# Performance work log

Hardware: AMD Instinct MI355X
Metric: run time of the kernel (lower is better)

Reference implementation:

```python
import jax, jax.numpy as jnp
import numpy as np

B, T, S = 256, 32, 128
I, H, O = 256, 1024, 256


def setup_inputs() -> dict:
    key = jax.random.key(0)
    ks = jax.random.split(key, 8)
    sc = 0.02
    return {
        "shifted_target": jax.random.normal(ks[0], (B, T, I), jnp.float32),
        "encoder_outputs": jax.random.normal(ks[1], (B, S, H), jnp.float32),
        "W_ih": jax.random.normal(ks[2], (4 * H, I), jnp.float32) * sc,
        "W_hh": jax.random.normal(ks[3], (4 * H, H), jnp.float32) * sc,
        "b_ih": jax.random.normal(ks[4], (4 * H,), jnp.float32) * sc,
        "b_hh": jax.random.normal(ks[5], (4 * H,), jnp.float32) * sc,
        "W_fc": jax.random.normal(ks[6], (O, 2 * H), jnp.float32) * sc,
        "b_fc": jax.random.normal(ks[7], (O,), jnp.float32) * sc,
    }


def reference(shifted_target, encoder_outputs, W_ih, W_hh, b_ih, b_hh, W_fc, b_fc):
    bs, tgt_len, inp = shifted_target.shape
    hid = encoder_outputs.shape[-1]
    # torch code feeds zeros (not shifted_target[:,0]) at t=0, with zero init state
    xs = shifted_target.at[:, 0, :].set(0.0)
    xs = jnp.swapaxes(xs, 0, 1)  # [T, B, I]

    def step(carry, x_t):
        h, c = carry
        gates = x_t @ W_ih.T + b_ih + h @ W_hh.T + b_hh  # [B, 4H]
        i, f, g, o = jnp.split(gates, 4, axis=-1)
        i = jax.nn.sigmoid(i)
        f = jax.nn.sigmoid(f)
        g = jnp.tanh(g)
        o = jax.nn.sigmoid(o)
        c = f * c + i * g
        h = o * jnp.tanh(c)
        # dot-product attention against encoder states
        score = jnp.einsum('bh,bsh->bs', h, encoder_outputs)
        prob = jax.nn.softmax(score, axis=-1)
        ctx = jnp.einsum('bs,bsh->bh', prob, encoder_outputs)
        out_t = jnp.concatenate([ctx, h], axis=-1) @ W_fc.T + b_fc
        return (h, c), (out_t, prob)

    h0 = jnp.zeros((bs, hid), shifted_target.dtype)
    c0 = jnp.zeros((bs, hid), shifted_target.dtype)
    _, (outs, probs) = jax.lax.scan(step, (h0, c0), xs)
    return jnp.swapaxes(outs, 0, 1), jnp.swapaxes(probs, 0, 1)
```

## Files before the change

kernel.cpp:

```cpp
#include <hip/hip_runtime.h>
#include <math.h>

#define B_  256
#define T_  32
#define S_  128
#define I_  256
#define H_  1024
#define O_  256
#define G4  4096
#define K2  2048

typedef __attribute__((ext_vector_type(8))) short bf16x8;
typedef __attribute__((ext_vector_type(4))) float f32x4;

#define MFMA16(a, b, c) __builtin_amdgcn_mfma_f32_16x16x32_bf16(a, b, c, 0, 0, 0)

__device__ __forceinline__ unsigned short f2bf(float f) {
    unsigned int u = __float_as_uint(f);
    u = (u + 0x7FFFu + ((u >> 16) & 1u)) >> 16;
    return (unsigned short)u;
}
__device__ __forceinline__ unsigned int pack2(float a, float b) {
    return (unsigned int)f2bf(a) | ((unsigned int)f2bf(b) << 16);
}
__device__ __forceinline__ float sigm(float x) { return 1.0f / (1.0f + __expf(-x)); }

__global__ void prep_kernel(
    const float* __restrict__ x, const float* __restrict__ Wih,
    const float* __restrict__ Whh, const float* __restrict__ bih,
    const float* __restrict__ bhh, const float* __restrict__ Wfc,
    unsigned short* __restrict__ WihR, unsigned short* __restrict__ WhhR,
    unsigned short* __restrict__ WfcR, float* __restrict__ biasR,
    unsigned short* __restrict__ xs, unsigned short* __restrict__ h0,
    unsigned short* __restrict__ h1, float* __restrict__ c)
{
    const long NWHH = (long)G4 * H_;
    const long NWIH = (long)G4 * I_;
    const long NWFC = (long)O_ * K2;
    const long NB   = G4;
    const long NX   = (long)B_ * T_ * I_;
    const long NH   = (long)B_ * H_;
    const long total = NWHH + NWIH + NWFC + NB + NX + 3 * NH;
    for (long i = (long)blockIdx.x * blockDim.x + threadIdx.x; i < total;
         i += (long)gridDim.x * blockDim.x) {
        long j = i;
        if (j < NWHH) {
            int r = (int)(j >> 10), k = (int)(j & 1023);
            int n = ((r & 1023) << 2) | (r >> 10);
            WhhR[(long)n * H_ + k] = f2bf(Whh[j]);
            continue;
        }
        j -= NWHH;
        if (j < NWIH) {
            int r = (int)(j >> 8), k = (int)(j & 255);
            int n = ((r & 1023) << 2) | (r >> 10);
            WihR[(long)n * I_ + k] = f2bf(Wih[j]);
            continue;
        }
        j -= NWIH;
        if (j < NWFC) { WfcR[j] = f2bf(Wfc[j]); continue; }
        j -= NWFC;
        if (j < NB) {
            int r = (int)j;
            int n = ((r & 1023) << 2) | (r >> 10);
            biasR[n] = bih[r] + bhh[r];
            continue;
        }
        j -= NB;
        if (j < NX) {
            int t = (int)((j >> 8) & 31);
            xs[j] = (t == 0) ? (unsigned short)0 : f2bf(x[j]);
            continue;
        }
        j -= NX;
        if (j < NH) { h0[j] = 0; continue; }
        j -= NH;
        if (j < NH) { h1[j] = 0; continue; }
        j -= NH;
        c[j] = 0.0f;
    }
}

__global__ __launch_bounds__(256) void step_kernel(
    const unsigned short* __restrict__ xs,
    const unsigned short* __restrict__ WihR,
    const unsigned short* __restrict__ WhhR,
    const float* __restrict__ biasR,
    const unsigned short* __restrict__ hprev,
    unsigned short* __restrict__ hnext,
    float* __restrict__ c,
    unsigned short* __restrict__ hall,
    int t)
{
    __shared__ __align__(16) char smem[64 * 132 * 4];
    unsigned short* As = (unsigned short*)smem;
    unsigned short* Bs = (unsigned short*)(smem + 64 * 40 * 2);
    float* Gs = (float*)smem;

    const int tid = threadIdx.x;
    const int lane = tid & 63, wave = tid >> 6;
    const int wm = wave >> 1, wn = wave & 1;
    const int quad = lane >> 4, l16 = lane & 15;
    const int n0 = blockIdx.x * 128, m0 = blockIdx.y * 64;

    const int arow = tid >> 2, akc = (tid & 3) * 8;
    const int brow = tid >> 1, bkc = (tid & 1) * 16;

    f32x4 acc[2][4];
    const f32x4 z = {0.f, 0.f, 0.f, 0.f};
#pragma unroll
    for (int i = 0; i < 2; i++)
#pragma unroll
        for (int j = 0; j < 4; j++) acc[i][j] = z;

    for (int k0 = 0; k0 < I_ + H_; k0 += 32) {
        {
            int kg = k0 + akc;
            const unsigned short* src = (kg < I_)
                ? xs + ((long)(m0 + arow) * T_ + t) * I_ + kg
                : hprev + (long)(m0 + arow) * H_ + (kg - I_);
            *(uint4*)(As + arow * 40 + akc) = *(const uint4*)src;
        }
        {
            int kg = k0 + bkc;
            const unsigned short* src = (kg < I_)
                ? WihR + (long)(n0 + brow) * I_ + kg
                : WhhR + (long)(n0 + brow) * H_ + (kg - I_);
            *(uint4*)(Bs + brow * 40 + bkc)     = *(const uint4*)src;
            *(uint4*)(Bs + brow * 40 + bkc + 8) = *(const uint4*)(src + 8);
        }
        __syncthreads();
        bf16x8 a0 = *(const bf16x8*)(As + (wm * 32 + l16) * 40 + quad * 8);
        bf16x8 a1 = *(const bf16x8*)(As + (wm * 32 + 16 + l16) * 40 + quad * 8);
#pragma unroll
        for (int j = 0; j < 4; j++) {
            bf16x8 bb = *(const bf16x8*)(Bs + (wn * 64 + j * 16 + l16) * 40 + quad * 8);
            acc[0][j] = MFMA16(a0, bb, acc[0][j]);
            acc[1][j] = MFMA16(a1, bb, acc[1][j]);
        }
        __syncthreads();
    }
#pragma unroll
    for (int i = 0; i < 2; i++)
#pragma unroll
        for (int j = 0; j < 4; j++)
#pragma unroll
            for (int r = 0; r < 4; r++) {
                int row = wm * 32 + i * 16 + quad * 4 + r;
                int col = wn * 64 + j * 16 + l16;
                Gs[row * 132 + col] = acc[i][j][r] + biasR[n0 + col];
            }
    __syncthreads();
    for (int p = tid; p < 2048; p += 256) {
        int row = p >> 5, u = p & 31;
        float gi = Gs[row * 132 + u * 4 + 0];
        float gf = Gs[row * 132 + u * 4 + 1];
        float gg = Gs[row * 132 + u * 4 + 2];
        float go = Gs[row * 132 + u * 4 + 3];
        int b = m0 + row;
        int jg = (n0 >> 2) + u;
        float ii = sigm(gi), ff = sigm(gf), g3 = tanhf(gg), oo = sigm(go);
        float cn = ff * c[(long)b * H_ + jg] + ii * g3;
        float hh = oo * tanhf(cn);
        c[(long)b * H_ + jg] = cn;
        unsigned short hb = f2bf(hh);
        hnext[(long)b * H_ + jg] = hb;
        hall[((long)b * T_ + t) * H_ + jg] = hb;
    }
}

__global__ __launch_bounds__(256) void attn_kernel(
    const float* __restrict__ enc,
    const unsigned short* __restrict__ hall,
    float* __restrict__ probs,
    unsigned short* __restrict__ cat)
{
    __shared__ __align__(16) unsigned short As2[32 * 72];
    __shared__ __align__(16) unsigned short Bs2[128 * 72];
    __shared__ __align__(16) float Sc[32 * 132];

    const int tid = threadIdx.x;
    const int lane = tid & 63, wave = tid >> 6;
    const int mw = wave & 1, nw = wave >> 1;
    const int quad = lane >> 4, l16 = lane & 15;
    const int b = blockIdx.x;

    f32x4 acc[4];
    const f32x4 z = {0.f, 0.f, 0.f, 0.f};
#pragma unroll
    for (int j = 0; j < 4; j++) acc[j] = z;

    const int arow = tid >> 3, akc = (tid & 7) * 8;
    const int brow = tid >> 1, bkc = (tid & 1) * 32;

    for (int k0 = 0; k0 < H_; k0 += 64) {
        *(uint4*)(As2 + arow * 72 + akc) =
            *(const uint4*)(hall + ((long)b * T_ + arow) * H_ + k0 + akc);
        {
            const float* ep = enc + ((long)b * S_ + brow) * H_ + k0 + bkc;
#pragma unroll
            for (int i = 0; i < 4; i++) {
                float4 f0 = *(const float4*)(ep + i * 8);
                float4 f1 = *(const float4*)(ep + i * 8 + 4);
                uint4 v;
                v.x = pack2(f0.x, f0.y);
                v.y = pack2(f0.z, f0.w);
                v.z = pack2(f1.x, f1.y);
                v.w = pack2(f1.z, f1.w);
                *(uint4*)(Bs2 + brow * 72 + bkc + i * 8) = v;
            }
        }
        __syncthreads();
#pragma unroll
        for (int ks = 0; ks < 2; ks++) {
            bf16x8 a = *(const bf16x8*)(As2 + (mw * 16 + l16) * 72 + ks * 32 + quad * 8);
#pragma unroll
            for (int j = 0; j < 4; j++) {
                bf16x8 bb = *(const bf16x8*)(Bs2 + (nw * 64 + j * 16 + l16) * 72 + ks * 32 + quad * 8);
                acc[j] = MFMA16(a, bb, acc[j]);
            }
        }
        __syncthreads();
    }
#pragma unroll
    for (int j = 0; j < 4; j++)
#pragma unroll
        for (int r = 0; r < 4; r++)
            Sc[(mw * 16 + quad * 4 + r) * 132 + nw * 64 + j * 16 + l16] = acc[j][r];
    __syncthreads();
    for (int r = 0; r < 8; r++) {
        int row = wave * 8 + r;
        float v0 = Sc[row * 132 + lane];
        float v1 = Sc[row * 132 + 64 + lane];
        float mx = fmaxf(v0, v1);
#pragma unroll
        for (int off = 32; off > 0; off >>= 1) mx = fmaxf(mx, __shfl_xor(mx, off));
        float e0 = __expf(v0 - mx), e1 = __expf(v1 - mx);
        float s = e0 + e1;
#pragma unroll
        for (int off = 32; off > 0; off >>= 1) s += __shfl_xor(s, off);
        float inv = 1.0f / s;
        float p0 = e0 * inv, p1 = e1 * inv;
        probs[((long)b * T_ + row) * S_ + lane] = p0;
        probs[((long)b * T_ + row) * S_ + 64 + lane] = p1;
        Sc[row * 132 + lane] = p0;
        Sc[row * 132 + 64 + lane] = p1;
    }
    __syncthreads();
    float ax[32], ay[32], az[32], aw[32];
#pragma unroll
    for (int t2 = 0; t2 < 32; t2++) { ax[t2] = 0; ay[t2] = 0; az[t2] = 0; aw[t2] = 0; }
    const float* ep0 = enc + (long)b * S_ * H_ + tid * 4;
    for (int s = 0; s < S_; s++) {
        float4 e = *(const float4*)(ep0 + (long)s * H_);
#pragma unroll
        for (int t2 = 0; t2 < 32; t2++) {
            float p = Sc[t2 * 132 + s];
            ax[t2] += p * e.x; ay[t2] += p * e.y;
            az[t2] += p * e.z; aw[t2] += p * e.w;
        }
    }
#pragma unroll
    for (int t2 = 0; t2 < 32; t2++) {
        uint2 v;
        v.x = pack2(ax[t2], ay[t2]);
        v.y = pack2(az[t2], aw[t2]);
        *(uint2*)(cat + ((long)(b * T_ + t2)) * K2 + tid * 4) = v;
    }
    const uint4* hs = (const uint4*)(hall + (long)b * T_ * H_);
    for (int i = tid; i < (T_ * H_) / 8; i += 256) {
        int t2 = i >> 7, cpos = i & 127;
        *(uint4*)(cat + ((long)(b * T_ + t2)) * K2 + H_ + cpos * 8) = hs[i];
    }
}

__global__ __launch_bounds__(256) void fc_kernel(
    const unsigned short* __restrict__ cat,
    const unsigned short* __restrict__ WfcR,
    const float* __restrict__ bfc,
    float* __restrict__ out)
{
    __shared__ __align__(16) unsigned short As[64 * 40];
    __shared__ __align__(16) unsigned short Bs[128 * 40];

    const int tid = threadIdx.x;
    const int lane = tid & 63, wave = tid >> 6;
    const int wm = wave >> 1, wn = wave & 1;
    const int quad = lane >> 4, l16 = lane & 15;
    const int n0 = blockIdx.x * 128, m0 = blockIdx.y * 64;

    const int arow = tid >> 2, akc = (tid & 3) * 8;
    const int brow = tid >> 1, bkc = (tid & 1) * 16;

    f32x4 acc[2][4];
    const f32x4 z = {0.f, 0.f, 0.f, 0.f};
#pragma unroll
    for (int i = 0; i < 2; i++)
#pragma unroll
        for (int j = 0; j < 4; j++) acc[i][j] = z;

    for (int k0 = 0; k0 < K2; k0 += 32) {
        *(uint4*)(As + arow * 40 + akc) =
            *(const uint4*)(cat + (long)(m0 + arow) * K2 + k0 + akc);
        const unsigned short* src = WfcR + (long)(n0 + brow) * K2 + k0 + bkc;
        *(uint4*)(Bs + brow * 40 + bkc)     = *(const uint4*)src;
        *(uint4*)(Bs + brow * 40 + bkc + 8) = *(const uint4*)(src + 8);
        __syncthreads();
        bf16x8 a0 = *(const bf16x8*)(As + (wm * 32 + l16) * 40 + quad * 8);
        bf16x8 a1 = *(const bf16x8*)(As + (wm * 32 + 16 + l16) * 40 + quad * 8);
#pragma unroll
        for (int j = 0; j < 4; j++) {
            bf16x8 bb = *(const bf16x8*)(Bs + (wn * 64 + j * 16 + l16) * 40 + quad * 8);
            acc[0][j] = MFMA16(a0, bb, acc[0][j]);
            acc[1][j] = MFMA16(a1, bb, acc[1][j]);
        }
        __syncthreads();
    }
#pragma unroll
    for (int i = 0; i < 2; i++)
#pragma unroll
        for (int j = 0; j < 4; j++)
#pragma unroll
            for (int r = 0; r < 4; r++) {
                int row = m0 + wm * 32 + i * 16 + quad * 4 + r;
                int col = n0 + wn * 64 + j * 16 + l16;
                out[(long)row * O_ + col] = acc[i][j][r] + bfc[col];
            }
}

extern "C" void kernel_launch(void* const* d_in, const int* in_sizes, int n_in,
                              void* d_out, int out_size, void* d_ws, size_t ws_size,
                              hipStream_t stream) {
    const float* x   = (const float*)d_in[0];
    const float* enc = (const float*)d_in[1];
    const float* Wih = (const float*)d_in[2];
    const float* Whh = (const float*)d_in[3];
    const float* bih = (const float*)d_in[4];
    const float* bhh = (const float*)d_in[5];
    const float* Wfc = (const float*)d_in[6];
    const float* bfc = (const float*)d_in[7];
    float* out = (float*)d_out;

    char* ws = (char*)d_ws;
    unsigned short* WIHR = (unsigned short*)(ws + 0);
    unsigned short* WHHR = (unsigned short*)(ws + 2097152);
    unsigned short* WFCR = (unsigned short*)(ws + 10485760);
    float*          BIAS = (float*)         (ws + 11534336);
    unsigned short* XS   = (unsigned short*)(ws + 11550720);
    unsigned short* H0   = (unsigned short*)(ws + 15745024);
    unsigned short* H1   = (unsigned short*)(ws + 16269312);
    float*          C    = (float*)         (ws + 16793600);
    unsigned short* HALL = (unsigned short*)(ws + 17842176);
    unsigned short* CAT  = (unsigned short*)(ws + 34619392);

    prep_kernel<<<4096, 256, 0, stream>>>(x, Wih, Whh, bih, bhh, Wfc,
                                          WIHR, WHHR, WFCR, BIAS, XS, H0, H1, C);

    for (int t = 0; t < T_; t++) {
        const unsigned short* hp = (t & 1) ? H1 : H0;
        unsigned short* hn = (t & 1) ? H0 : H1;
        step_kernel<<<dim3(32, 4), 256, 0, stream>>>(XS, WIHR, WHHR, BIAS,
                                                     hp, hn, C, HALL, t);
    }

    attn_kernel<<<B_, 256, 0, stream>>>(enc, HALL, out + (long)B_ * T_ * O_, CAT);
    fc_kernel<<<dim3(2, 128), 256, 0, stream>>>(CAT, WFCR, bfc, out);
}
```

Measured before the change: 1.156 ms.

## Rework step GEMM to direct-load MFMA and split attention into MFMA kernels

The per-timestep LSTM gate GEMM drops its LDS staging and barriers: each wave now loads bf16 fragments straight from global memory, and tiles shrink to 64 columns so the grid doubles to 256 blocks. Encoder outputs are converted to bf16 once in the prep kernel. Attention is split into a scores+softmax kernel and a context kernel; the context product now uses MFMA instead of a scalar FP32 loop, with probabilities stored in bf16. The concat buffer is gone, and the FC kernel reads ctx and hall directly. The cost is an extra full pass over the encoder for conversion, a large new bf16 encoder buffer, and strided scalar LDS reads when building the context B fragments.

```diff
diff --git a/kernel.cpp b/kernel.cpp
--- a/kernel.cpp
+++ b/kernel.cpp
@@ -20,30 +20,32 @@
     u = (u + 0x7FFFu + ((u >> 16) & 1u)) >> 16;
     return (unsigned short)u;
 }
-__device__ __forceinline__ unsigned int pack2(float a, float b) {
-    return (unsigned int)f2bf(a) | ((unsigned int)f2bf(b) << 16);
-}
 __device__ __forceinline__ float sigm(float x) { return 1.0f / (1.0f + __expf(-x)); }
 
 __global__ void prep_kernel(
-    const float* __restrict__ x, const float* __restrict__ Wih,
-    const float* __restrict__ Whh, const float* __restrict__ bih,
-    const float* __restrict__ bhh, const float* __restrict__ Wfc,
+    const float* __restrict__ x, const float* __restrict__ enc,
+    const float* __restrict__ Wih, const float* __restrict__ Whh,
+    const float* __restrict__ bih, const float* __restrict__ bhh,
+    const float* __restrict__ Wfc,
     unsigned short* __restrict__ WihR, unsigned short* __restrict__ WhhR,
     unsigned short* __restrict__ WfcR, float* __restrict__ biasR,
-    unsigned short* __restrict__ xs, unsigned short* __restrict__ h0,
-    unsigned short* __restrict__ h1, float* __restrict__ c)
+    unsigned short* __restrict__ xs, unsigned short* __restrict__ encB,
+    unsigned short* __restrict__ h0, unsigned short* __restrict__ h1,
+    float* __restrict__ c)
 {
     const long NWHH = (long)G4 * H_;
     const long NWIH = (long)G4 * I_;
     const long NWFC = (long)O_ * K2;
     const long NB   = G4;
     const long NX   = (long)B_ * T_ * I_;
+    const long NE   = (long)B_ * S_ * H_;
     const long NH   = (long)B_ * H_;
-    const long total = NWHH + NWIH + NWFC + NB + NX + 3 * NH;
+    const long total = NWHH + NWIH + NWFC + NB + NX + NE + 3 * NH;
     for (long i = (long)blockIdx.x * blockDim.x + threadIdx.x; i < total;
          i += (long)gridDim.x * blockDim.x) {
         long j = i;
+        if (j < NE) { encB[j] = f2bf(enc[j]); continue; }
+        j -= NE;
         if (j < NWHH) {
             int r = (int)(j >> 10), k = (int)(j & 1023);
             int n = ((r & 1023) << 2) | (r >> 10);
@@ -92,71 +94,72 @@
     unsigned short* __restrict__ hall,
     int t)
 {
-    __shared__ __align__(16) char smem[64 * 132 * 4];
-    unsigned short* As = (unsigned short*)smem;
-    unsigned short* Bs = (unsigned short*)(smem + 64 * 40 * 2);
-    float* Gs = (float*)smem;
+    __shared__ float Gs[64 * 68];
 
     const int tid = threadIdx.x;
     const int lane = tid & 63, wave = tid >> 6;
     const int wm = wave >> 1, wn = wave & 1;
     const int quad = lane >> 4, l16 = lane & 15;
-    const int n0 = blockIdx.x * 128, m0 = blockIdx.y * 64;
-
-    const int arow = tid >> 2, akc = (tid & 3) * 8;
-    const int brow = tid >> 1, bkc = (tid & 1) * 16;
-
-    f32x4 acc[2][4];
+    const int n0 = blockIdx.x * 64, m0 = blockIdx.y * 64;
+
+    const int ar0 = m0 + wm * 32 + l16, ar1 = ar0 + 16;
+    const int br0 = n0 + wn * 32 + l16, br1 = br0 + 16;
+
+    const unsigned short* ax0 = xs + ((long)ar0 * T_ + t) * I_ + quad * 8;
+    const unsigned short* ax1 = xs + ((long)ar1 * T_ + t) * I_ + quad * 8;
+    const unsigned short* ah0 = hprev + (long)ar0 * H_ + quad * 8;
+    const unsigned short* ah1 = hprev + (long)ar1 * H_ + quad * 8;
+    const unsigned short* bx0 = WihR + (long)br0 * I_ + quad * 8;
+    const unsigned short* bx1 = WihR + (long)br1 * I_ + quad * 8;
+    const unsigned short* bh0 = WhhR + (long)br0 * H_ + quad * 8;
+    const unsigned short* bh1 = WhhR + (long)br1 * H_ + quad * 8;
+
     const f32x4 z = {0.f, 0.f, 0.f, 0.f};
-#pragma unroll
-    for (int i = 0; i < 2; i++)
-#pragma unroll
-        for (int j = 0; j < 4; j++) acc[i][j] = z;
-
-    for (int k0 = 0; k0 < I_ + H_; k0 += 32) {
-        {
-            int kg = k0 + akc;
-            const unsigned short* src = (kg < I_)
-                ? xs + ((long)(m0 + arow) * T_ + t) * I_ + kg
-                : hprev + (long)(m0 + arow) * H_ + (kg - I_);
-            *(uint4*)(As + arow * 40 + akc) = *(const uint4*)src;
-        }
-        {
-            int kg = k0 + bkc;
-            const unsigned short* src = (kg < I_)
-                ? WihR + (long)(n0 + brow) * I_ + kg
-                : WhhR + (long)(n0 + brow) * H_ + (kg - I_);
-            *(uint4*)(Bs + brow * 40 + bkc)     = *(const uint4*)src;
-            *(uint4*)(Bs + brow * 40 + bkc + 8) = *(const uint4*)(src + 8);
-        }
-        __syncthreads();
-        bf16x8 a0 = *(const bf16x8*)(As + (wm * 32 + l16) * 40 + quad * 8);
-        bf16x8 a1 = *(const bf16x8*)(As + (wm * 32 + 16 + l16) * 40 + quad * 8);
-#pragma unroll
-        for (int j = 0; j < 4; j++) {
-            bf16x8 bb = *(const bf16x8*)(Bs + (wn * 64 + j * 16 + l16) * 40 + quad * 8);
-            acc[0][j] = MFMA16(a0, bb, acc[0][j]);
-            acc[1][j] = MFMA16(a1, bb, acc[1][j]);
-        }
-        __syncthreads();
-    }
-#pragma unroll
-    for (int i = 0; i < 2; i++)
-#pragma unroll
-        for (int j = 0; j < 4; j++)
-#pragma unroll
-            for (int r = 0; r < 4; r++) {
-                int row = wm * 32 + i * 16 + quad * 4 + r;
-                int col = wn * 64 + j * 16 + l16;
-                Gs[row * 132 + col] = acc[i][j][r] + biasR[n0 + col];
-            }
+    f32x4 acc00 = z, acc01 = z, acc10 = z, acc11 = z;
+
+#pragma unroll
+    for (int k0 = 0; k0 < I_; k0 += 32) {
+        bf16x8 a0 = *(const bf16x8*)(ax0 + k0);
+        bf16x8 a1 = *(const bf16x8*)(ax1 + k0);
+        bf16x8 b0 = *(const bf16x8*)(bx0 + k0);
+        bf16x8 b1 = *(const bf16x8*)(bx1 + k0);
+        acc00 = MFMA16(a0, b0, acc00);
+        acc01 = MFMA16(a0, b1, acc01);
+        acc10 = MFMA16(a1, b0, acc10);
+        acc11 = MFMA16(a1, b1, acc11);
+    }
+#pragma unroll 4
+    for (int k0 = 0; k0 < H_; k0 += 32) {
+        bf16x8 a0 = *(const bf16x8*)(ah0 + k0);
+        bf16x8 a1 = *(const bf16x8*)(ah1 + k0);
+        bf16x8 b0 = *(const bf16x8*)(bh0 + k0);
+        bf16x8 b1 = *(const bf16x8*)(bh1 + k0);
+        acc00 = MFMA16(a0, b0, acc00);
+        acc01 = MFMA16(a0, b1, acc01);
+        acc10 = MFMA16(a1, b0, acc10);
+        acc11 = MFMA16(a1, b1, acc11);
+    }
+
+    const float bj0 = biasR[n0 + wn * 32 + l16];
+    const float bj1 = biasR[n0 + wn * 32 + 16 + l16];
+#pragma unroll
+    for (int r = 0; r < 4; r++) {
+        int row0 = wm * 32 + quad * 4 + r;
+        int col0 = wn * 32 + l16;
+        Gs[row0 * 68 + col0]            = acc00[r] + bj0;
+        Gs[row0 * 68 + col0 + 16]       = acc01[r] + bj1;
+        Gs[(row0 + 16) * 68 + col0]      = acc10[r] + bj0;
+        Gs[(row0 + 16) * 68 + col0 + 16] = acc11[r] + bj1;
+    }
     __syncthreads();
-    for (int p = tid; p < 2048; p += 256) {
-        int row = p >> 5, u = p & 31;
-        float gi = Gs[row * 132 + u * 4 + 0];
-        float gf = Gs[row * 132 + u * 4 + 1];
-        float gg = Gs[row * 132 + u * 4 + 2];
-        float go = Gs[row * 132 + u * 4 + 3];
+
+#pragma unroll
+    for (int p = tid; p < 1024; p += 256) {
+        int row = p >> 4, u = p & 15;
+        float gi = Gs[row * 68 + u * 4 + 0];
+        float gf = Gs[row * 68 + u * 4 + 1];
+        float gg = Gs[row * 68 + u * 4 + 2];
+        float go = Gs[row * 68 + u * 4 + 3];
         int b = m0 + row;
         int jg = (n0 >> 2) + u;
         float ii = sigm(gi), ff = sigm(gf), g3 = tanhf(gg), oo = sigm(go);
@@ -169,64 +172,48 @@
     }
 }
 
-__global__ __launch_bounds__(256) void attn_kernel(
-    const float* __restrict__ enc,
+__global__ __launch_bounds__(256) void scores_kernel(
     const unsigned short* __restrict__ hall,
+    const unsigned short* __restrict__ encB,
     float* __restrict__ probs,
-    unsigned short* __restrict__ cat)
-{
-    __shared__ __align__(16) unsigned short As2[32 * 72];
-    __shared__ __align__(16) unsigned short Bs2[128 * 72];
-    __shared__ __align__(16) float Sc[32 * 132];
+    unsigned short* __restrict__ PB)
+{
+    __shared__ float Sc[32 * 132];
 
     const int tid = threadIdx.x;
     const int lane = tid & 63, wave = tid >> 6;
-    const int mw = wave & 1, nw = wave >> 1;
     const int quad = lane >> 4, l16 = lane & 15;
     const int b = blockIdx.x;
-
-    f32x4 acc[4];
+    const int nw = wave;
+
+    const unsigned short* pa0 = hall + ((long)b * T_ + l16) * H_ + quad * 8;
+    const unsigned short* pa1 = hall + ((long)b * T_ + 16 + l16) * H_ + quad * 8;
+    const unsigned short* pb0 = encB + ((long)b * S_ + nw * 32 + l16) * H_ + quad * 8;
+    const unsigned short* pb1 = pb0 + 16 * H_;
+
     const f32x4 z = {0.f, 0.f, 0.f, 0.f};
-#pragma unroll
-    for (int j = 0; j < 4; j++) acc[j] = z;
-
-    const int arow = tid >> 3, akc = (tid & 7) * 8;
-    const int brow = tid >> 1, bkc = (tid & 1) * 32;
-
-    for (int k0 = 0; k0 < H_; k0 += 64) {
-        *(uint4*)(As2 + arow * 72 + akc) =
-            *(const uint4*)(hall + ((long)b * T_ + arow) * H_ + k0 + akc);
-        {
-            const float* ep = enc + ((long)b * S_ + brow) * H_ + k0 + bkc;
-#pragma unroll
-            for (int i = 0; i < 4; i++) {
-                float4 f0 = *(const float4*)(ep + i * 8);
-                float4 f1 = *(const float4*)(ep + i * 8 + 4);
-                uint4 v;
-                v.x = pack2(f0.x, f0.y);
-                v.y = pack2(f0.z, f0.w);
-                v.z = pack2(f1.x, f1.y);
-                v.w = pack2(f1.z, f1.w);
-                *(uint4*)(Bs2 + brow * 72 + bkc + i * 8) = v;
-            }
-        }
-        __syncthreads();
-#pragma unroll
-        for (int ks = 0; ks < 2; ks++) {
-            bf16x8 a = *(const bf16x8*)(As2 + (mw * 16 + l16) * 72 + ks * 32 + quad * 8);
-#pragma unroll
-            for (int j = 0; j < 4; j++) {
-                bf16x8 bb = *(const bf16x8*)(Bs2 + (nw * 64 + j * 16 + l16) * 72 + ks * 32 + quad * 8);
-                acc[j] = MFMA16(a, bb, acc[j]);
-            }
-        }
-        __syncthreads();
-    }
-#pragma unroll
-    for (int j = 0; j < 4; j++)
-#pragma unroll
-        for (int r = 0; r < 4; r++)
-            Sc[(mw * 16 + quad * 4 + r) * 132 + nw * 64 + j * 16 + l16] = acc[j][r];
+    f32x4 acc00 = z, acc01 = z, acc10 = z, acc11 = z;
+
+#pragma unroll 4
+    for (int k0 = 0; k0 < H_; k0 += 32) {
+        bf16x8 a0 = *(const bf16x8*)(pa0 + k0);
+        bf16x8 a1 = *(const bf16x8*)(pa1 + k0);
+        bf16x8 b0 = *(const bf16x8*)(pb0 + k0);
+        bf16x8 b1 = *(const bf16x8*)(pb1 + k0);
+        acc00 = MFMA16(a0, b0, acc00);
+        acc01 = MFMA16(a0, b1, acc01);
+        acc10 = MFMA16(a1, b0, acc10);
+        acc11 = MFMA16(a1, b1, acc11);
+    }
+#pragma unroll
+    for (int r = 0; r < 4; r++) {
+        int row0 = quad * 4 + r;
+        int col0 = nw * 32 + l16;
+        Sc[row0 * 132 + col0]            = acc00[r];
+        Sc[row0 * 132 + col0 + 16]       = acc01[r];
+        Sc[(row0 + 16) * 132 + col0]      = acc10[r];
+        Sc[(row0 + 16) * 132 + col0 + 16] = acc11[r];
+    }
     __syncthreads();
     for (int r = 0; r < 8; r++) {
         int row = wave * 8 + r;
@@ -241,41 +228,77 @@
         for (int off = 32; off > 0; off >>= 1) s += __shfl_xor(s, off);
         float inv = 1.0f / s;
         float p0 = e0 * inv, p1 = e1 * inv;
-        probs[((long)b * T_ + row) * S_ + lane] = p0;
-        probs[((long)b * T_ + row) * S_ + 64 + lane] = p1;
-        Sc[row * 132 + lane] = p0;
-        Sc[row * 132 + 64 + lane] = p1;
-    }
+        long o = ((long)b * T_ + row) * S_;
+        probs[o + lane] = p0;
+        probs[o + 64 + lane] = p1;
+        PB[o + lane] = f2bf(p0);
+        PB[o + 64 + lane] = f2bf(p1);
+    }
+}
+
+__global__ __launch_bounds__(256) void ctx_kernel(
+    const unsigned short* __restrict__ encB,
+    const unsigned short* __restrict__ PB,
+    unsigned short* __restrict__ ctxo)
+{
+    __shared__ unsigned short Es[S_ * 256];
+
+    const int tid = threadIdx.x;
+    const int lane = tid & 63, wave = tid >> 6;
+    const int quad = lane >> 4, l16 = lane & 15;
+    const int b = blockIdx.x;
+    const int h0 = blockIdx.y * 256;
+
+    for (int i = tid; i < S_ * 32; i += 256) {
+        int s = i >> 5, hc = (i & 31) * 8;
+        *(uint4*)(Es + s * 256 + hc) =
+            *(const uint4*)(encB + ((long)b * S_ + s) * H_ + h0 + hc);
+    }
+    bf16x8 a[2][4];
+#pragma unroll
+    for (int i = 0; i < 2; i++)
+#pragma unroll
+        for (int ks = 0; ks < 4; ks++)
+            a[i][ks] = *(const bf16x8*)(PB + ((long)b * T_ + i * 16 + l16) * S_ +
+                                        ks * 32 + quad * 8);
     __syncthreads();
-    float ax[32], ay[32], az[32], aw[32];
-#pragma unroll
-    for (int t2 = 0; t2 < 32; t2++) { ax[t2] = 0; ay[t2] = 0; az[t2] = 0; aw[t2] = 0; }
-    const float* ep0 = enc + (long)b * S_ * H_ + tid * 4;
-    for (int s = 0; s < S_; s++) {
-        float4 e = *(const float4*)(ep0 + (long)s * H_);
-#pragma unroll
-        for (int t2 = 0; t2 < 32; t2++) {
-            float p = Sc[t2 * 132 + s];
-            ax[t2] += p * e.x; ay[t2] += p * e.y;
-            az[t2] += p * e.z; aw[t2] += p * e.w;
-        }
-    }
-#pragma unroll
-    for (int t2 = 0; t2 < 32; t2++) {
-        uint2 v;
-        v.x = pack2(ax[t2], ay[t2]);
-        v.y = pack2(az[t2], aw[t2]);
-        *(uint2*)(cat + ((long)(b * T_ + t2)) * K2 + tid * 4) = v;
-    }
-    const uint4* hs = (const uint4*)(hall + (long)b * T_ * H_);
-    for (int i = tid; i < (T_ * H_) / 8; i += 256) {
-        int t2 = i >> 7, cpos = i & 127;
-        *(uint4*)(cat + ((long)(b * T_ + t2)) * K2 + H_ + cpos * 8) = hs[i];
-    }
+
+    f32x4 acc[2][4];
+    const f32x4 z = {0.f, 0.f, 0.f, 0.f};
+#pragma unroll
+    for (int i = 0; i < 2; i++)
+#pragma unroll
+        for (int j = 0; j < 4; j++) acc[i][j] = z;
+
+    const int cw = wave * 64;
+#pragma unroll
+    for (int ks = 0; ks < 4; ks++) {
+        const int kb = ks * 32 + quad * 8;
+#pragma unroll
+        for (int j = 0; j < 4; j++) {
+            const int col = cw + j * 16 + l16;
+            bf16x8 bb;
+#pragma unroll
+            for (int e = 0; e < 8; e++) bb[e] = (short)Es[(kb + e) * 256 + col];
+            acc[0][j] = MFMA16(a[0][ks], bb, acc[0][j]);
+            acc[1][j] = MFMA16(a[1][ks], bb, acc[1][j]);
+        }
+    }
+#pragma unroll
+    for (int i = 0; i < 2; i++)
+#pragma unroll
+        for (int j = 0; j < 4; j++)
+#pragma unroll
+            for (int r = 0; r < 4; r++) {
+                int row = i * 16 + quad * 4 + r;
+                int col = h0 + cw + j * 16 + l16;
+                ctxo[((long)b * T_ + row) * H_ + col] = f2bf(acc[i][j][r]);
+            }
 }
 
 __global__ __launch_bounds__(256) void fc_kernel(
-    const unsigned short* __restrict__ cat,
+    const unsigned short* __restrict__ ctxo,
+    const unsigned short* __restrict__ hall,
     const unsigned short* __restrict__ WfcR,
     const float* __restrict__ bfc,
     float* __restrict__ out)
@@ -300,8 +323,10 @@
         for (int j = 0; j < 4; j++) acc[i][j] = z;
 
     for (int k0 = 0; k0 < K2; k0 += 32) {
-        *(uint4*)(As + arow * 40 + akc) =
-            *(const uint4*)(cat + (long)(m0 + arow) * K2 + k0 + akc);
+        const unsigned short* asrc = (k0 < H_)
+            ? ctxo + (long)(m0 + arow) * H_ + k0 + akc
+            : hall + (long)(m0 + arow) * H_ + (k0 - H_) + akc;
+        *(uint4*)(As + arow * 40 + akc) = *(const uint4*)asrc;
         const unsigned short* src = WfcR + (long)(n0 + brow) * K2 + k0 + bkc;
         *(uint4*)(Bs + brow * 40 + bkc)     = *(const uint4*)src;
         *(uint4*)(Bs + brow * 40 + bkc + 8) = *(const uint4*)(src + 8);
@@ -351,18 +376,23 @@
     unsigned short* H1   = (unsigned short*)(ws + 16269312);
     float*          C    = (float*)         (ws + 16793600);
     unsigned short* HALL = (unsigned short*)(ws + 17842176);
-    unsigned short* CAT  = (unsigned short*)(ws + 34619392);
-
-    prep_kernel<<<4096, 256, 0, stream>>>(x, Wih, Whh, bih, bhh, Wfc,
-                                          WIHR, WHHR, WFCR, BIAS, XS, H0, H1, C);
+    unsigned short* ENCB = (unsigned short*)(ws + 34619392);
+    unsigned short* PB   = (unsigned short*)(ws + 101728256);
+    unsigned short* CTX  = (unsigned short*)(ws + 103825408);
+
+    prep_kernel<<<8192, 256, 0, stream>>>(x, enc, Wih, Whh, bih, bhh, Wfc,
+                                          WIHR, WHHR, WFCR, BIAS, XS, ENCB,
+                                          H0, H1, C);
 
     for (int t = 0; t < T_; t++) {
         const unsigned short* hp = (t & 1) ? H1 : H0;
         unsigned short* hn = (t & 1) ? H0 : H1;
-        step_kernel<<<dim3(32, 4), 256, 0, stream>>>(XS, WIHR, WHHR, BIAS,
+        step_kernel<<<dim3(64, 4), 256, 0, stream>>>(XS, WIHR, WHHR, BIAS,
                                                      hp, hn, C, HALL, t);
     }
 
-    attn_kernel<<<B_, 256, 0, stream>>>(enc, HALL, out + (long)B_ * T_ * O_, CAT);
-    fc_kernel<<<dim3(2, 128), 256, 0, stream>>>(CAT, WFCR, bfc, out);
-}
+    scores_kernel<<<B_, 256, 0, stream>>>(HALL, ENCB,
+                                          out + (long)B_ * T_ * O_, PB);
+    ctx_kernel<<<dim3(B_, 4), 256, 0, stream>>>(ENCB, PB, CTX);
+    fc_kernel<<<dim3(2, 128), 256, 0, stream>>>(CTX, HALL, WFCR, bfc, out);
+}
```

Measured after the change: 1.113 ms. -3.7%, faster.
